# Kernel tuning notes

Measured on AMD Instinct MI355X. Metric: run time of the kernel, lower is better.

## Reference

```python
import jax, jax.numpy as jnp
import numpy as np

N = 100000   # nodes
E = 1600000  # edges (avg degree 16)
G = 128      # graphs in batch
D_IN, D_HID, D_OUT = 128, 256, 128


def setup_inputs() -> dict:
    key = jax.random.key(0)
    ks = jax.random.split(key, 12)
    x = jax.random.normal(ks[0], (N, D_IN), jnp.float32)
    edge_index = jax.random.randint(ks[1], (2, E), 0, N, dtype=jnp.int64)
    batch = jnp.sort(jax.random.randint(ks[2], (N,), 0, G, dtype=jnp.int64))

    def lin(k, i, o):
        return jax.random.normal(k, (i, o), jnp.float32) / np.float32(np.sqrt(i))

    return {
        "x": x, "edge_index": edge_index, "batch": batch,
        "W0": lin(ks[3], D_IN, D_HID),  "b0": jnp.zeros((D_HID,), jnp.float32),
        "W1": lin(ks[4], D_HID, D_HID), "b1": jnp.zeros((D_HID,), jnp.float32),
        "W2": lin(ks[5], D_HID, D_OUT), "b2": jnp.zeros((D_OUT,), jnp.float32),
        "Wf1": lin(ks[6], D_OUT, D_HID), "bf1": jnp.zeros((D_HID,), jnp.float32),
        "Wf2": lin(ks[7], D_HID, 1),     "bf2": jnp.zeros((1,), jnp.float32),
    }


def reference(x, edge_index, batch, W0, b0, W1, b1, W2, b2, Wf1, bf1, Wf2, bf2):
    n = x.shape[0]
    # GCNConv: add self-loops, symmetric deg^{-1/2} normalization,
    # linear transform, scatter-add aggregation, bias added after aggregation
    # (matches PyG GCNConv defaults; dropout is identity in eval mode).
    loop = jnp.arange(n, dtype=edge_index.dtype)
    src = jnp.concatenate([edge_index[0], loop])
    dst = jnp.concatenate([edge_index[1], loop])
    deg = jax.ops.segment_sum(jnp.ones_like(dst, x.dtype), dst, num_segments=n)
    dinv = jax.lax.rsqrt(jnp.maximum(deg, 1.0))  # deg >= 1 after self-loops
    norm = dinv[src] * dinv[dst]                 # [E+N]

    def conv(h, W, b):
        h = h @ W                                # [N, out]
        msg = h[src] * norm[:, None]             # gather + normalize
        return jax.ops.segment_sum(msg, dst, num_segments=n) + b

    h = jax.nn.relu(conv(x, W0, b0))
    h = jax.nn.relu(conv(h, W1, b1))
    h = conv(h, W2, b2)                          # last conv, no relu

    # global mean pool over graphs
    s = jax.ops.segment_sum(h, batch, num_segments=G)
    cnt = jax.ops.segment_sum(jnp.ones((n,), h.dtype), batch, num_segments=G)
    g = s / jnp.maximum(cnt, 1.0)[:, None]       # [G, D_OUT]

    out = jax.nn.relu(g @ Wf1 + bf1)
    return jax.nn.sigmoid(out @ Wf2 + bf2)       # [G, 1]
```

## Files before the change

### kernel.cpp

```cpp
#include <hip/hip_runtime.h>
#include <hip/hip_bf16.h>

typedef __hip_bfloat16 hbf16;
typedef __attribute__((ext_vector_type(8))) short short8;
typedef __attribute__((ext_vector_type(4))) float f32x4;
typedef __attribute__((ext_vector_type(2))) float f32x2;
typedef __attribute__((ext_vector_type(4))) float f32x4v;

static __device__ __forceinline__ float bits2f(unsigned short u) {
  return __uint_as_float(((unsigned)u) << 16);
}
static __device__ __forceinline__ unsigned short f2bits(float f) {
  hbf16 h = __float2bfloat16(f);
  return *reinterpret_cast<unsigned short*>(&h);
}


#define BSH2 9
#define CHUNK 8192

__global__ __launch_bounds__(256) void k_bcnt(
    const int* __restrict__ dst, int e, int nbuk,
    int* __restrict__ bcnt, int* __restrict__ blockOff) {
  __shared__ int hist[1024];
  int t = threadIdx.x;
  int e0 = blockIdx.x * CHUNK;
  int e1 = min(e, e0 + CHUNK);
  for (int b = t; b < nbuk; b += 256) hist[b] = 0;
  __syncthreads();
  for (int i = e0 + t; i < e1; i += 256)
    atomicAdd(&hist[__builtin_nontemporal_load(&dst[i]) >> BSH2], 1);
  __syncthreads();
  for (int b = t; b < nbuk; b += 256) {
    int h = hist[b];
    blockOff[(size_t)blockIdx.x * nbuk + b] = h ? atomicAdd(&bcnt[b], h) : 0;
  }
}

__global__ __launch_bounds__(1024) void k_scanB(
    const int* __restrict__ bcnt, int nbuk, int e,
    int* __restrict__ bstart, int* __restrict__ rowStart, int n) {
  __shared__ int s[1024];
  int t = threadIdx.x;
  int v = (t < nbuk) ? bcnt[t] : 0;
  s[t] = v;
  __syncthreads();
  for (int off = 1; off < 1024; off <<= 1) {
    int x = (t >= off) ? s[t - off] : 0;
    __syncthreads();
    s[t] += x;
    __syncthreads();
  }
  if (t < nbuk) bstart[t] = s[t] - v;
  if (t == 0) { bstart[nbuk] = e; rowStart[n] = e; }
}

__global__ __launch_bounds__(256) void k_partA(
    const int* __restrict__ src, const int* __restrict__ dst, int e, int nbuk,
    const int* __restrict__ bstart, const int* __restrict__ blockOff,
    unsigned* __restrict__ staging) {
  __shared__ int pos[1024];
  int t = threadIdx.x;
  int e0 = blockIdx.x * CHUNK;
  int e1 = min(e, e0 + CHUNK);
  for (int b = t; b < nbuk; b += 256)
    pos[b] = bstart[b] + blockOff[(size_t)blockIdx.x * nbuk + b];
  __syncthreads();
  for (int i = e0 + t; i < e1; i += 256) {
    int d = __builtin_nontemporal_load(&dst[i]);
    int sv = __builtin_nontemporal_load(&src[i]);
    int b = d >> BSH2;
    int r = atomicAdd(&pos[b], 1);
    staging[r] = (unsigned)sv | ((unsigned)(d & 511) << 23);
  }
}

__global__ __launch_bounds__(512) void k_bucket_csr(
    const unsigned* __restrict__ staging, const int* __restrict__ bstart,
    int* __restrict__ rowStart, float* __restrict__ dinv, int* __restrict__ csr, int N) {
  __shared__ int hist[512];
  __shared__ int s[512];
  __shared__ int cnt[512];
  int b = blockIdx.x, t = threadIdx.x;
  int es = bstart[b], ee = bstart[b + 1];
  hist[t] = 0;
  __syncthreads();
  for (int i = es + t; i < ee; i += 512)
    atomicAdd(&hist[staging[i] >> 23], 1);
  __syncthreads();
  s[t] = hist[t];
  __syncthreads();
  for (int off = 1; off < 512; off <<= 1) {
    int x = (t >= off) ? s[t - off] : 0;
    __syncthreads();
    s[t] += x;
    __syncthreads();
  }
  int gpos = es + s[t] - hist[t];
  cnt[t] = gpos;
  int d = (b << BSH2) + t;
  if (d < N) {
    rowStart[d] = gpos;
    dinv[d] = rsqrtf((float)(hist[t] + 1));
  }
  __syncthreads();
  for (int i = es + t; i < ee; i += 512) {
    unsigned w = staging[i];
    int pos = atomicAdd(&cnt[w >> 23], 1);
    csr[pos] = (int)(w & 0x7fffffu);
  }
}

__global__ void k_wt_all(const float* __restrict__ W0, const float* __restrict__ W1,
                         const float* __restrict__ W2, unsigned short* __restrict__ W0t,
                         unsigned short* __restrict__ W1t, unsigned short* __restrict__ W2t) {
  int i = blockIdx.x * blockDim.x + threadIdx.x;
  const float* W; unsigned short* Wt; int K, M, idx;
  if (i < 32768)       { W = W0; Wt = W0t; K = 128; M = 256; idx = i; }
  else if (i < 98304)  { W = W1; Wt = W1t; K = 256; M = 256; idx = i - 32768; }
  else if (i < 131072) { W = W2; Wt = W2t; K = 256; M = 128; idx = i - 98304; }
  else return;
  int m = idx / K, k = idx - m * K;
  Wt[idx] = f2bits(W[k * M + m]);
}

__global__ void k_cast_fp8(const float* __restrict__ x, const float* __restrict__ dinv,
                           unsigned* __restrict__ y, int n4) {
  int i = blockIdx.x * blockDim.x + threadIdx.x;
  if (i < n4) {
    float s = 16.f * dinv[i >> 5];
    f32x4v v = __builtin_nontemporal_load(reinterpret_cast<const f32x4v*>(x) + i);
    unsigned q = 0;
    q = __builtin_amdgcn_cvt_pk_fp8_f32(v[0] * s, v[1] * s, q, false);
    q = __builtin_amdgcn_cvt_pk_fp8_f32(v[2] * s, v[3] * s, q, true);
    y[i] = q;
  }
}


template<int VPL>
static __device__ __forceinline__ unsigned agg8_load(
    const void* __restrict__ h8, int idx, int lane) {
  if constexpr (VPL == 4)
    return reinterpret_cast<const unsigned*>(h8)[(size_t)idx * 64 + lane];
  else
    return (unsigned)reinterpret_cast<const unsigned short*>(h8)[(size_t)idx * 64 + lane];
}

template<int VPL>
static __device__ __forceinline__ void agg8_add(unsigned v, float* acc) {
  f32x2 lo = __builtin_amdgcn_cvt_pk_f32_fp8(v, false);
  acc[0] += lo[0]; acc[1] += lo[1];
  if constexpr (VPL == 4) {
    f32x2 hi = __builtin_amdgcn_cvt_pk_f32_fp8(v, true);
    acc[2] += hi[0]; acc[3] += hi[1];
  }
}

template<int VPL, int U>
static __device__ __forceinline__ void agg8_chunk(
    const void* __restrict__ h8, const int* __restrict__ csr,
    int k, int lane, float* acc) {
  unsigned v[U];
#pragma unroll
  for (int u = 0; u < U; ++u) {
    int idx = __builtin_nontemporal_load(&csr[k + u]);
    v[u] = agg8_load<VPL>(h8, idx, lane);
  }
#pragma unroll
  for (int u = 0; u < U; ++u) agg8_add<VPL>(v[u], acc);
}

template<int D, int BIAS>
__global__ __launch_bounds__(256) void aggregate_f8(
    const void* __restrict__ h8, const int* __restrict__ csr,
    const int* __restrict__ rowStart, const float* __restrict__ dinv,
    const float* __restrict__ bias, void* __restrict__ outv, int N) {
  constexpr int VPL = D / 64;
  int lane = threadIdx.x & 63;
  int d = (blockIdx.x * 256 + threadIdx.x) >> 6;
  if (d >= N) return;
  int rs = __builtin_amdgcn_readfirstlane(rowStart[d]);
  int re = __builtin_amdgcn_readfirstlane(rowStart[d + 1]);

  float acc[VPL] = {};
  agg8_add<VPL>(agg8_load<VPL>(h8, d, lane), acc);

  int k = rs;
  for (; k + 16 <= re; k += 16) agg8_chunk<VPL, 16>(h8, csr, k, lane, acc);
  if (k + 8 <= re) { agg8_chunk<VPL, 8>(h8, csr, k, lane, acc); k += 8; }
  if (k + 4 <= re) { agg8_chunk<VPL, 4>(h8, csr, k, lane, acc); k += 4; }
  for (; k < re; ++k) {
    int idx = __builtin_nontemporal_load(&csr[k]);
    agg8_add<VPL>(agg8_load<VPL>(h8, idx, lane), acc);
  }

  float dv = dinv[d];
  float v[VPL];
#pragma unroll
  for (int j = 0; j < VPL; ++j) {
    v[j] = acc[j] * dv;
    if (BIAS) v[j] += 16.f * bias[lane * VPL + j];
  }
  if constexpr (VPL == 4) {
    unsigned q = 0;
    q = __builtin_amdgcn_cvt_pk_fp8_f32(v[0], v[1], q, false);
    q = __builtin_amdgcn_cvt_pk_fp8_f32(v[2], v[3], q, true);
    reinterpret_cast<unsigned*>(outv)[(size_t)d * 64 + lane] = q;
  } else {
    unsigned q = __builtin_amdgcn_cvt_pk_fp8_f32(v[0], v[1], 0, false);
    reinterpret_cast<unsigned short*>(outv)[(size_t)d * 64 + lane] = (unsigned short)q;
  }
}


#define GLD16(g, l) __builtin_amdgcn_global_load_lds(                         \
    (const __attribute__((address_space(1))) void*)(g),                       \
    (__attribute__((address_space(3))) void*)(l), 16, 0, 0)

static __device__ __forceinline__ void dq_store(uint4 v, char* lA, int r, int c8) {
  unsigned ow[8];
#pragma unroll
  for (int j = 0; j < 4; ++j) {
    unsigned w = (&v.x)[j];
    f32x2 lo = __builtin_amdgcn_cvt_pk_f32_fp8(w, false);
    f32x2 hi = __builtin_amdgcn_cvt_pk_f32_fp8(w, true);
    ow[2 * j]     = (unsigned)f2bits(lo[0]) | ((unsigned)f2bits(lo[1]) << 16);
    ow[2 * j + 1] = (unsigned)f2bits(hi[0]) | ((unsigned)f2bits(hi[1]) << 16);
  }
  int s0 = (c8 * 2) ^ (r & 7);
  int s1 = (c8 * 2 + 1) ^ (r & 7);
  *reinterpret_cast<uint4*>(lA + r * 128 + s0 * 16) = make_uint4(ow[0], ow[1], ow[2], ow[3]);
  *reinterpret_cast<uint4*>(lA + r * 128 + s1 * 16) = make_uint4(ow[4], ow[5], ow[6], ow[7]);
}

template<int K, int EPI>
__global__ __launch_bounds__(256) void gemm_mfma(
    const unsigned char* __restrict__ A8, const unsigned short* __restrict__ Bt,
    const float* __restrict__ bias, const float* __restrict__ dinv,
    unsigned char* __restrict__ C8, int N, int M) {
  __shared__ __align__(16) char smem[32768];
  char* lA = smem;
  char* lB = smem + 16384;
  int tid = threadIdx.x, lane = tid & 63, wid = tid >> 6;
  int rowBase = blockIdx.x * 128, colBase = blockIdx.y * 128;
  int wr = (wid >> 1) * 64, wc = (wid & 1) * 64;

  f32x4 zero = {0.f, 0.f, 0.f, 0.f};
  f32x4 acc[4][4];
#pragma unroll
  for (int m = 0; m < 4; ++m)
#pragma unroll
    for (int n = 0; n < 4; ++n) acc[m][n] = zero;

  const char* Bb = (const char*)Bt;
  int ar = tid >> 1, ah = tid & 1;
  int ga = min(rowBase + ar, N - 1);

  for (int k0 = 0; k0 < K; k0 += 64) {
#pragma unroll
    for (int r = 0; r < 4; ++r) {
      int pbase = r * 256 + wid * 64;
      int p = pbase + lane;
      int row = p >> 3;
      int offg = ((p & 7) * 16) ^ ((row & 7) << 4);
      int gb = colBase + row;
      GLD16(Bb + (size_t)gb * (K * 2) + k0 * 2 + offg, lB + pbase * 16);
    }
    {
      const unsigned char* Ap = A8 + (size_t)ga * K + k0 + ah * 32;
      uint4 va = *reinterpret_cast<const uint4*>(Ap);
      uint4 vb = *reinterpret_cast<const uint4*>(Ap + 16);
      dq_store(va, lA, ar, ah * 2);
      dq_store(vb, lA, ar, ah * 2 + 1);
    }
    __syncthreads();
    int l15 = lane & 15, lhi = lane >> 4;
#pragma unroll
    for (int kk = 0; kk < 2; ++kk) {
      short8 af[4], bfr[4];
      int koff = kk * 64 + lhi * 16;
#pragma unroll
      for (int m = 0; m < 4; ++m) {
        int row = wr + m * 16 + l15;
        af[m] = *reinterpret_cast<const short8*>(lA + row * 128 + (koff ^ ((row & 7) << 4)));
      }
#pragma unroll
      for (int n = 0; n < 4; ++n) {
        int col = wc + n * 16 + l15;
        bfr[n] = *reinterpret_cast<const short8*>(lB + col * 128 + (koff ^ ((col & 7) << 4)));
      }
#pragma unroll
      for (int m = 0; m < 4; ++m)
#pragma unroll
        for (int n = 0; n < 4; ++n)
          acc[m][n] = __builtin_amdgcn_mfma_f32_16x16x32_bf16(bfr[n], af[m], acc[m][n], 0, 0, 0);
    }
    __syncthreads();
  }

  int l15 = lane & 15, lhi = lane >> 4;
#pragma unroll
  for (int m = 0; m < 4; ++m) {
    int row = rowBase + wr + m * 16 + l15;
    if (row >= N) continue;
    float dq = 1.f;
    if (EPI == 2) dq = 16.f * dinv[row];
    else if (EPI == 3) dq = dinv[row];
#pragma unroll
    for (int n = 0; n < 4; ++n) {
      int col = colBase + wc + n * 16 + lhi * 4;
      float4 bv4 = make_float4(0.f, 0.f, 0.f, 0.f);
      if (EPI == 2 || EPI == 4) bv4 = *reinterpret_cast<const float4*>(bias + col);
      float v[4];
#pragma unroll
      for (int j = 0; j < 4; ++j) {
        float a16 = acc[m][n][j];
        float bj = (&bv4.x)[j];
        if (EPI == 2)      v[j] = fmaxf(fmaf(a16, 0.0625f, bj), 0.f) * dq;
        else if (EPI == 3) v[j] = a16 * dq;
        else               v[j] = fmaxf(a16 + 16.f * bj, 0.f);
      }
      unsigned q = 0;
      q = __builtin_amdgcn_cvt_pk_fp8_f32(v[0], v[1], q, false);
      q = __builtin_amdgcn_cvt_pk_fp8_f32(v[2], v[3], q, true);
      *reinterpret_cast<unsigned*>(C8 + (size_t)row * M + col) = q;
    }
  }
}


__global__ void graph_bounds(const int* batch, int n, int g_cnt, int* gstart) {
  int g = blockIdx.x * blockDim.x + threadIdx.x;
  if (g > g_cnt) return;
  int lo = 0, hi = n;
  while (lo < hi) {
    int mid = (lo + hi) >> 1;
    if (batch[mid] < g) lo = mid + 1; else hi = mid;
  }
  gstart[g] = lo;
}

__global__ void pool_partial(const unsigned char* __restrict__ h8,
                             const int* __restrict__ batch, int N, float* gbuf) {
  int per = (N + gridDim.x - 1) / gridDim.x;
  int lo = blockIdx.x * per;
  int hi = min(N, lo + per);
  if (lo >= hi) return;
  int t = threadIdx.x;
  int cur = batch[lo];
  float acc = 0.f;
  for (int i = lo; i < hi; ++i) {
    int g = batch[i];
    if (g != cur) {
      atomicAdd(&gbuf[cur * 128 + t], acc);
      acc = 0.f;
      cur = g;
    }
    unsigned b = (unsigned)__builtin_nontemporal_load(&h8[(size_t)i * 128 + t]);
    f32x2 lo2 = __builtin_amdgcn_cvt_pk_f32_fp8(b, false);
    acc += lo2[0];
  }
  atomicAdd(&gbuf[cur * 128 + t], acc);
}


__global__ __launch_bounds__(256) void mlp(const float* __restrict__ gbuf,
                                           const int* __restrict__ gstart,
                                           const float* __restrict__ Wf1,
                                           const float* __restrict__ bf1,
                                           const float* __restrict__ Wf2,
                                           const float* __restrict__ bf2,
                                           float* __restrict__ out) {
  __shared__ float gs[128];
  __shared__ float hid[256];
  int b = blockIdx.x, t = threadIdx.x;
  float inv = 0.0625f / (float)max(gstart[b + 1] - gstart[b], 1);
  if (t < 128) gs[t] = gbuf[b * 128 + t] * inv;
  __syncthreads();
  float acc = bf1[t];
  for (int k = 0; k < 128; ++k) acc += gs[k] * Wf1[k * 256 + t];
  acc = fmaxf(acc, 0.f);
  hid[t] = acc * Wf2[t];
  __syncthreads();
  for (int s2 = 128; s2 > 0; s2 >>= 1) {
    if (t < s2) hid[t] += hid[t + s2];
    __syncthreads();
  }
  if (t == 0) out[b] = 1.f / (1.f + expf(-(hid[0] + bf2[0])));
}


extern "C" void kernel_launch(void* const* d_in, const int* in_sizes, int n_in,
                              void* d_out, int out_size, void* d_ws, size_t ws_size,
                              hipStream_t stream) {
  const float* x   = (const float*)d_in[0];
  const int* ei    = (const int*)d_in[1];
  const int* batch = (const int*)d_in[2];
  const float* W0  = (const float*)d_in[3];
  const float* b0  = (const float*)d_in[4];
  const float* W1  = (const float*)d_in[5];
  const float* b1  = (const float*)d_in[6];
  const float* W2  = (const float*)d_in[7];
  const float* b2  = (const float*)d_in[8];
  const float* Wf1 = (const float*)d_in[9];
  const float* bf1 = (const float*)d_in[10];
  const float* Wf2 = (const float*)d_in[11];
  const float* bf2 = (const float*)d_in[12];
  float* out = (float*)d_out;

  const int DIN = 128, DH = 256, DOUT = 128, G = 128;
  const int N = in_sizes[0] / DIN;
  const int E = in_sizes[1] / 2;
  const int* src = ei;
  const int* dst = ei + E;
  const int NBUK = (N + 511) >> BSH2;
  const int NCHUNK = (E + CHUNK - 1) / CHUNK;

  char* p = (char*)d_ws;
  auto alloc = [&](size_t bytes) {
    char* r = p;
    p += (bytes + 255) & ~(size_t)255;
    return r;
  };
  int* bcnt     = (int*)alloc((size_t)NBUK * 4);
  int* blockOff = (int*)alloc((size_t)NCHUNK * NBUK * 4);
  int* bstart   = (int*)alloc((size_t)(NBUK + 1) * 4);
  int* rowStart = (int*)alloc((size_t)(N + 1) * 4);
  float* dinv   = (float*)alloc((size_t)N * 4);
  int* csr      = (int*)alloc((size_t)E * 4);
  int* gstart   = (int*)alloc((size_t)(G + 1) * 4);
  float* gbuf   = (float*)alloc((size_t)G * DOUT * 4);
  unsigned short* W0t = (unsigned short*)alloc((size_t)DIN * DH * 2);
  unsigned short* W1t = (unsigned short*)alloc((size_t)DH * DH * 2);
  unsigned short* W2t = (unsigned short*)alloc((size_t)DH * DOUT * 2);
  char* S1 = (char*)alloc((size_t)N * DH * 2);
  char* S2 = (char*)alloc((size_t)N * DH * 2);

  unsigned* staging = (unsigned*)S2;

  unsigned*      xb8     = (unsigned*)S1;
  unsigned char* agg0_8  = (unsigned char*)S2;
  unsigned char* h1s8    = (unsigned char*)S1;
  unsigned char* agg1_8  = (unsigned char*)S2;
  unsigned char* h2_8    = (unsigned char*)S1;
  unsigned char* t2s8    = (unsigned char*)S2;
  unsigned char* aggout8 = (unsigned char*)S1;

  const int tb = 256;
  hipMemsetAsync(bcnt, 0, (size_t)NBUK * 4, stream);
  hipMemsetAsync(gbuf, 0, (size_t)G * DOUT * 4, stream);

  k_bcnt<<<NCHUNK, 256, 0, stream>>>(dst, E, NBUK, bcnt, blockOff);
  k_scanB<<<1, 1024, 0, stream>>>(bcnt, NBUK, E, bstart, rowStart, N);
  k_partA<<<NCHUNK, 256, 0, stream>>>(src, dst, E, NBUK, bstart, blockOff, staging);
  k_bucket_csr<<<NBUK, 512, 0, stream>>>(staging, bstart, rowStart, dinv, csr, N);

  k_wt_all<<<(131072 + tb - 1) / tb, tb, 0, stream>>>(W0, W1, W2, W0t, W1t, W2t);

  int n4 = N * DIN / 4;
  k_cast_fp8<<<(n4 + tb - 1) / tb, tb, 0, stream>>>(x, dinv, xb8, n4);

  int gx = (N + 127) / 128;
  int ga = (N + 3) / 4;

  aggregate_f8<128, 0><<<ga, 256, 0, stream>>>(xb8, csr, rowStart, dinv, nullptr, agg0_8, N);
  gemm_mfma<128, 2><<<dim3(gx, 2), 256, 0, stream>>>(agg0_8, W0t, b0, dinv, h1s8, N, DH);

  aggregate_f8<256, 0><<<ga, 256, 0, stream>>>(h1s8, csr, rowStart, dinv, nullptr, agg1_8, N);
  gemm_mfma<256, 4><<<dim3(gx, 2), 256, 0, stream>>>(agg1_8, W1t, b1, nullptr, h2_8, N, DH);

  gemm_mfma<256, 3><<<dim3(gx, 1), 256, 0, stream>>>(h2_8, W2t, nullptr, dinv, t2s8, N, DOUT);
  aggregate_f8<128, 1><<<ga, 256, 0, stream>>>(t2s8, csr, rowStart, dinv, b2, aggout8, N);

  graph_bounds<<<1, 256, 0, stream>>>(batch, N, G, gstart);
  pool_partial<<<1000, 128, 0, stream>>>(aggout8, batch, N, gbuf);
  mlp<<<G, 256, 0, stream>>>(gbuf, gstart, Wf1, bf1, Wf2, bf2, out);
}
```

Before: 351.0 us.

## Remove memsets and small launches by restructuring bucket histogram scan

```diff
diff --git a/kernel.cpp b/kernel.cpp
--- a/kernel.cpp
+++ b/kernel.cpp
@@ -7,9 +7,6 @@
 typedef __attribute__((ext_vector_type(2))) float f32x2;
 typedef __attribute__((ext_vector_type(4))) float f32x4v;
 
-static __device__ __forceinline__ float bits2f(unsigned short u) {
-  return __uint_as_float(((unsigned)u) << 16);
-}
 static __device__ __forceinline__ unsigned short f2bits(float f) {
   hbf16 h = __float2bfloat16(f);
   return *reinterpret_cast<unsigned short*>(&h);
@@ -19,9 +16,8 @@
 #define BSH2 9
 #define CHUNK 8192
 
-__global__ __launch_bounds__(256) void k_bcnt(
-    const int* __restrict__ dst, int e, int nbuk,
-    int* __restrict__ bcnt, int* __restrict__ blockOff) {
+__global__ __launch_bounds__(256) void k_hist2d(
+    const int* __restrict__ dst, int e, int nbuk, int* __restrict__ hist2d) {
   __shared__ int hist[1024];
   int t = threadIdx.x;
   int e0 = blockIdx.x * CHUNK;
@@ -31,40 +27,46 @@
   for (int i = e0 + t; i < e1; i += 256)
     atomicAdd(&hist[__builtin_nontemporal_load(&dst[i]) >> BSH2], 1);
   __syncthreads();
-  for (int b = t; b < nbuk; b += 256) {
-    int h = hist[b];
-    blockOff[(size_t)blockIdx.x * nbuk + b] = h ? atomicAdd(&bcnt[b], h) : 0;
-  }
-}
-
-__global__ __launch_bounds__(1024) void k_scanB(
-    const int* __restrict__ bcnt, int nbuk, int e,
+  for (int b = t; b < nbuk; b += 256)
+    hist2d[(size_t)blockIdx.x * nbuk + b] = hist[b];
+}
+
+__global__ __launch_bounds__(256) void k_scanB2(
+    int* __restrict__ hist2d, int nchunk, int nbuk, int e,
     int* __restrict__ bstart, int* __restrict__ rowStart, int n) {
-  __shared__ int s[1024];
-  int t = threadIdx.x;
-  int v = (t < nbuk) ? bcnt[t] : 0;
-  s[t] = v;
-  __syncthreads();
-  for (int off = 1; off < 1024; off <<= 1) {
-    int x = (t >= off) ? s[t - off] : 0;
-    __syncthreads();
-    s[t] += x;
-    __syncthreads();
-  }
-  if (t < nbuk) bstart[t] = s[t] - v;
-  if (t == 0) { bstart[nbuk] = e; rowStart[n] = e; }
+  __shared__ int s[256];
+  int b = threadIdx.x;
+  int running = 0;
+  if (b < nbuk) {
+    for (int c = 0; c < nchunk; ++c) {
+      size_t idx = (size_t)c * nbuk + b;
+      int t = hist2d[idx];
+      hist2d[idx] = running;
+      running += t;
+    }
+  }
+  s[b] = (b < nbuk) ? running : 0;
+  __syncthreads();
+  for (int off = 1; off < 256; off <<= 1) {
+    int x = (b >= off) ? s[b - off] : 0;
+    __syncthreads();
+    s[b] += x;
+    __syncthreads();
+  }
+  if (b < nbuk) bstart[b] = s[b] - running;
+  if (b == 0) { bstart[nbuk] = e; rowStart[n] = e; }
 }
 
 __global__ __launch_bounds__(256) void k_partA(
     const int* __restrict__ src, const int* __restrict__ dst, int e, int nbuk,
-    const int* __restrict__ bstart, const int* __restrict__ blockOff,
+    const int* __restrict__ bstart, const int* __restrict__ hist2d,
     unsigned* __restrict__ staging) {
   __shared__ int pos[1024];
   int t = threadIdx.x;
   int e0 = blockIdx.x * CHUNK;
   int e1 = min(e, e0 + CHUNK);
   for (int b = t; b < nbuk; b += 256)
-    pos[b] = bstart[b] + blockOff[(size_t)blockIdx.x * nbuk + b];
+    pos[b] = bstart[b] + hist2d[(size_t)blockIdx.x * nbuk + b];
   __syncthreads();
   for (int i = e0 + t; i < e1; i += 256) {
     int d = __builtin_nontemporal_load(&dst[i]);
@@ -113,12 +115,14 @@
 
 __global__ void k_wt_all(const float* __restrict__ W0, const float* __restrict__ W1,
                          const float* __restrict__ W2, unsigned short* __restrict__ W0t,
-                         unsigned short* __restrict__ W1t, unsigned short* __restrict__ W2t) {
+                         unsigned short* __restrict__ W1t, unsigned short* __restrict__ W2t,
+                         float* __restrict__ gbuf) {
   int i = blockIdx.x * blockDim.x + threadIdx.x;
   const float* W; unsigned short* Wt; int K, M, idx;
   if (i < 32768)       { W = W0; Wt = W0t; K = 128; M = 256; idx = i; }
   else if (i < 98304)  { W = W1; Wt = W1t; K = 256; M = 256; idx = i - 32768; }
   else if (i < 131072) { W = W2; Wt = W2t; K = 256; M = 128; idx = i - 98304; }
+  else if (i < 147456) { gbuf[i - 131072] = 0.f; return; }
   else return;
   int m = idx / K, k = idx - m * K;
   Wt[idx] = f2bits(W[k * M + m]);
@@ -329,17 +333,6 @@
   }
 }
 
-
-__global__ void graph_bounds(const int* batch, int n, int g_cnt, int* gstart) {
-  int g = blockIdx.x * blockDim.x + threadIdx.x;
-  if (g > g_cnt) return;
-  int lo = 0, hi = n;
-  while (lo < hi) {
-    int mid = (lo + hi) >> 1;
-    if (batch[mid] < g) lo = mid + 1; else hi = mid;
-  }
-  gstart[g] = lo;
-}
 
 __global__ void pool_partial(const unsigned char* __restrict__ h8,
                              const int* __restrict__ batch, int N, float* gbuf) {
@@ -366,7 +359,7 @@
 
 
 __global__ __launch_bounds__(256) void mlp(const float* __restrict__ gbuf,
-                                           const int* __restrict__ gstart,
+                                           const int* __restrict__ batch, int N,
                                            const float* __restrict__ Wf1,
                                            const float* __restrict__ bf1,
                                            const float* __restrict__ Wf2,
@@ -374,8 +367,17 @@
                                            float* __restrict__ out) {
   __shared__ float gs[128];
   __shared__ float hid[256];
+  __shared__ int cnt_s;
   int b = blockIdx.x, t = threadIdx.x;
-  float inv = 0.0625f / (float)max(gstart[b + 1] - gstart[b], 1);
+  if (t == 0) {
+    int lo = 0, hi = N;
+    while (lo < hi) { int mid = (lo + hi) >> 1; if (batch[mid] < b) lo = mid + 1; else hi = mid; }
+    int l2 = lo, h2 = N;
+    while (l2 < h2) { int mid = (l2 + h2) >> 1; if (batch[mid] < b + 1) l2 = mid + 1; else h2 = mid; }
+    cnt_s = max(l2 - lo, 1);
+  }
+  __syncthreads();
+  float inv = 0.0625f / (float)cnt_s;
   if (t < 128) gs[t] = gbuf[b * 128 + t] * inv;
   __syncthreads();
   float acc = bf1[t];
@@ -423,13 +425,11 @@
     p += (bytes + 255) & ~(size_t)255;
     return r;
   };
-  int* bcnt     = (int*)alloc((size_t)NBUK * 4);
-  int* blockOff = (int*)alloc((size_t)NCHUNK * NBUK * 4);
+  int* hist2d   = (int*)alloc((size_t)NCHUNK * NBUK * 4);
   int* bstart   = (int*)alloc((size_t)(NBUK + 1) * 4);
   int* rowStart = (int*)alloc((size_t)(N + 1) * 4);
   float* dinv   = (float*)alloc((size_t)N * 4);
   int* csr      = (int*)alloc((size_t)E * 4);
-  int* gstart   = (int*)alloc((size_t)(G + 1) * 4);
   float* gbuf   = (float*)alloc((size_t)G * DOUT * 4);
   unsigned short* W0t = (unsigned short*)alloc((size_t)DIN * DH * 2);
   unsigned short* W1t = (unsigned short*)alloc((size_t)DH * DH * 2);
@@ -448,15 +448,13 @@
   unsigned char* aggout8 = (unsigned char*)S1;
 
   const int tb = 256;
-  hipMemsetAsync(bcnt, 0, (size_t)NBUK * 4, stream);
-  hipMemsetAsync(gbuf, 0, (size_t)G * DOUT * 4, stream);
-
-  k_bcnt<<<NCHUNK, 256, 0, stream>>>(dst, E, NBUK, bcnt, blockOff);
-  k_scanB<<<1, 1024, 0, stream>>>(bcnt, NBUK, E, bstart, rowStart, N);
-  k_partA<<<NCHUNK, 256, 0, stream>>>(src, dst, E, NBUK, bstart, blockOff, staging);
+
+  k_hist2d<<<NCHUNK, 256, 0, stream>>>(dst, E, NBUK, hist2d);
+  k_scanB2<<<1, 256, 0, stream>>>(hist2d, NCHUNK, NBUK, E, bstart, rowStart, N);
+  k_partA<<<NCHUNK, 256, 0, stream>>>(src, dst, E, NBUK, bstart, hist2d, staging);
   k_bucket_csr<<<NBUK, 512, 0, stream>>>(staging, bstart, rowStart, dinv, csr, N);
 
-  k_wt_all<<<(131072 + tb - 1) / tb, tb, 0, stream>>>(W0, W1, W2, W0t, W1t, W2t);
+  k_wt_all<<<(147456 + tb - 1) / tb, tb, 0, stream>>>(W0, W1, W2, W0t, W1t, W2t, gbuf);
 
   int n4 = N * DIN / 4;
   k_cast_fp8<<<(n4 + tb - 1) / tb, tb, 0, stream>>>(x, dinv, xb8, n4);
@@ -473,7 +471,6 @@
   gemm_mfma<256, 3><<<dim3(gx, 1), 256, 0, stream>>>(h2_8, W2t, nullptr, dinv, t2s8, N, DOUT);
   aggregate_f8<128, 1><<<ga, 256, 0, stream>>>(t2s8, csr, rowStart, dinv, b2, aggout8, N);
 
-  graph_bounds<<<1, 256, 0, stream>>>(batch, N, G, gstart);
   pool_partial<<<1000, 128, 0, stream>>>(aggout8, batch, N, gbuf);
-  mlp<<<G, 256, 0, stream>>>(gbuf, gstart, Wf1, bf1, Wf2, bf2, out);
-}
+  mlp<<<G, 256, 0, stream>>>(gbuf, batch, N, Wf1, bf1, Wf2, bf2, out);
+}
```

Measured after the change: 386.0 us. 1.1x slower.
